# Kernel optimization log

Hardware: AMD Instinct MI355X
Metric: run time of the kernel (lower is better)

## Reference

```python
import jax, jax.numpy as jnp
import numpy as np

MARGIN = 1.0
REL_W = 0.3


def setup_inputs() -> dict:
    key = jax.random.key(0)
    ks = jax.random.split(key, 12)
    D = 256
    inp = {
        'support': jax.random.normal(ks[0], (16, 5, 1, 2, D), jnp.float32),
        'support_negative': jax.random.normal(ks[1], (16, 5, 1, 2, D), jnp.float32),
        'query': jax.random.normal(ks[2], (16, 128, 1, 2, D), jnp.float32),
        'negative': jax.random.normal(ks[3], (16, 128, 1, 2, D), jnp.float32),
        # PatternLearner conv weights (kaiming-ish scale), squeezed to 2-D since all convs are (1,3)/(1,1)
        'w1': jax.random.normal(ks[4], (128, 3), jnp.float32) * np.float32(np.sqrt(2.0 / 3.0)),
        'b1': jnp.zeros((128,), jnp.float32),
        'w2': jax.random.normal(ks[5], (64, 128), jnp.float32) * np.float32(np.sqrt(2.0 / 128.0)),
        'b2': jnp.zeros((64,), jnp.float32),
        'w3': jax.random.normal(ks[6], (32, 64), jnp.float32) * np.float32(np.sqrt(2.0 / 64.0)),
        'b3': jnp.zeros((32,), jnp.float32),
        'w4': jax.random.normal(ks[7], (1, 32), jnp.float32) * np.float32(np.sqrt(2.0 / 32.0)),
        'b4': jnp.zeros((1,), jnp.float32),
    }
    return inp


def _pattern_learner(x, w1, b1, w2, b2, w3, b3, w4, b4):
    # x: [B, N, 1, 3, D] -> torch does view+transpose -> conv2d(1,3) over the length-3 axis,
    # then 1x1 channel convs; equivalent to per-(n,d) contractions.
    h = x[:, :, 0]                                   # [B, N, 3, D]
    h = jnp.einsum('bnld,ol->bndo', h, w1) + b1      # [B, N, D, 128]
    h = jax.nn.relu(h)
    h = jax.nn.relu(jnp.einsum('bndi,oi->bndo', h, w2) + b2)
    h = jax.nn.relu(jnp.einsum('bndi,oi->bndo', h, w3) + b3)
    h = jnp.einsum('bndi,oi->bndo', h, w4) + b4      # [B, N, D, 1]
    return h[..., 0]                                 # [B, N, D]


def _concat_relation(pairs, rel):
    # pairs: [B, N, 1, 2, D]; rel: [B, 1, 1, 1, D]
    B, N, C, _, D = pairs.shape
    head = pairs[:, :, :, 0, :]
    tail = pairs[:, :, :, 1, :]
    relb = jnp.broadcast_to(rel[:, :, :, 0, :], (B, N, C, D))
    # torch cat order (relation, head, tail) then reindex [1,0,2] -> (head, relation, tail)
    return jnp.stack([head, relb, tail], axis=3)     # [B, N, 1, 3, D]


def _pattern_match(q, s):
    # q: [B, Nq, D], s: [B, 1, D] -> -L2 norm
    return -jnp.linalg.norm(q - s, axis=-1)


def reference(support, support_negative, query, negative, w1, b1, w2, b2, w3, b3, w4, b4):
    B, num_q = query.shape[0], query.shape[1]
    num_n = negative.shape[1]
    # get_relation(mean=True): tail - head averaged over the few support pairs
    rel = jnp.mean(support[:, :, :, 1, :] - support[:, :, :, 0, :], axis=1, keepdims=True)
    rel = rel[:, :, :, None, :]                      # [B, 1, 1, 1, D]

    sup_t = _concat_relation(support, rel)
    supn_t = _concat_relation(support_negative, rel)
    qry_t = _concat_relation(query, rel)
    neg_t = _concat_relation(negative, rel)

    pl = lambda x: _pattern_learner(x, w1, b1, w2, b2, w3, b3, w4, b4)
    spt_pos = pl(sup_t)                              # [B, few, D]
    spt_neg = pl(supn_t)                             # [B, num_sn, D]
    qry = pl(jnp.concatenate([qry_t, neg_t], axis=1))  # [B, num_q+num_n, D]

    # aggregator == 'relation': prototypes are per-task means of positive support patterns
    proto = jnp.mean(spt_pos, axis=1)                # [B, D]
    spt_pos_m = proto[:, None, :]                    # [B, 1, D]
    spt_neg_m = jnp.mean(spt_neg, axis=1, keepdims=True)

    qry_pos = _pattern_match(qry, spt_pos_m)         # [B, Nq]
    qry_neg = _pattern_match(qry, spt_neg_m)

    # relation_score (vectorized): mean L2 distance to all OTHER tasks' prototypes, negated
    dists = jnp.linalg.norm(qry[:, :, None, :] - proto[None, None, :, :], axis=-1)  # [B, Nq, B]
    idx = jnp.arange(B)
    self_d = dists[idx, :, idx]                      # [B, Nq]
    relation_score = -(dists.sum(-1) - self_d) / (B - 1)

    # margin loss on the true-query slice
    pos_score = _pattern_match(qry[:, :num_q], spt_pos_m)
    neg_score = _pattern_match(qry[:, :num_q], spt_neg_m)
    pos_ = jnp.mean(pos_score)
    neg_ = jnp.mean(neg_score)
    delta_loss = jnp.maximum(0.0, pos_ - neg_ + MARGIN)

    score = jnp.stack([qry_pos, qry_neg], axis=-1).reshape(-1, 2)
    row = jnp.concatenate([jnp.zeros((num_q,), jnp.int32), jnp.ones((num_n,), jnp.int32)])
    y_query = jnp.broadcast_to(row, (B, num_q + num_n)).reshape(-1)

    delta = qry_pos - qry_neg - REL_W * relation_score  # vbm + relation branch
    p_score = delta[:, :num_q]
    n_score = delta[:, num_q:]
    return (score, y_query, p_score, n_score, delta_loss)
```

## Files before the change

### kernel.cpp

```cpp
#include <hip/hip_runtime.h>
#include <hip/hip_bf16.h>

typedef _Float16 f16;
typedef f16 f16x8 __attribute__((ext_vector_type(8)));
typedef f16 f16x2 __attribute__((ext_vector_type(2)));
typedef float f32x4 __attribute__((ext_vector_type(4)));
typedef unsigned int u32;

#define MFMA16(a, b, c) __builtin_amdgcn_mfma_f32_16x16x32_f16((a), (b), (c), 0, 0, 0)

__device__ __forceinline__ u32 pkrz(float a, float b) {
    auto r = __builtin_amdgcn_cvt_pkrtz(a, b);
    return __builtin_bit_cast(u32, r);
}
__device__ __forceinline__ u32 pkmax0(u32 x) {
    f16x2 h = __builtin_bit_cast(f16x2, x);
    f16x2 z = {(f16)0.f, (f16)0.f};
    f16x2 m = __builtin_elementwise_max(h, z);
    return __builtin_bit_cast(u32, m);
}
__device__ __forceinline__ u32 pkrelu(float a, float b) {
    return pkmax0(pkrz(a, b));
}

union U8 { f16x8 h; u32 w[4]; };

#define OFF_Y      4096
#define OFF_PROTO  1093632
#define OFF_SNEG   1097728

__device__ __forceinline__ int b_of(int e) {
    if (e < 20480) return e / 1280;
    if (e < 40960) return (e - 20480) / 1280;
    return (e - 40960) >> 16;
}

__global__ __launch_bounds__(256, 2) void k_main(
    const float* __restrict__ sup, const float* __restrict__ supn,
    const float* __restrict__ qry, const float* __restrict__ neg,
    const float* __restrict__ w1, const float* __restrict__ b1p,
    const float* __restrict__ w2, const float* __restrict__ w3,
    const float* __restrict__ w4, const float* __restrict__ b2p,
    const float* __restrict__ b3p, const float* __restrict__ b4p,
    float* __restrict__ ws)
{
    __shared__ __align__(16) f16x8 w2lds[16 * 64];
    __shared__ __align__(16) f16x8 wpk[13 * 64];
    __shared__ uint2 stage[4][64];
    __shared__ float relb[2][256];
    float* wsY = ws + OFF_Y;

    int tid = threadIdx.x, wv = tid >> 6, lane = tid & 63;
    int g = lane >> 4, col = lane & 15;
    const f32x4 zero4 = {0.f, 0.f, 0.f, 0.f};

    int blkbase = blockIdx.x * 1024;
    int rb0 = b_of(blkbase), rb1 = b_of(blkbase + 1023);

    #pragma unroll
    for (int k = 0; k < 2; k++) {
        int bb = k ? rb1 : rb0;
        float acc = 0.f;
        #pragma unroll
        for (int n = 0; n < 5; n++) {
            const float* base = sup + ((bb * 5 + n) * 2) * 256 + tid;
            acc += base[256] - base[0];
        }
        relb[k][tid] = acc * 0.2f;
    }

    #pragma unroll
    for (int i = 0; i < 4; i++) {
        int id = tid + 256 * i;
        int f = id >> 6, ln = id & 63;
        int gg = ln >> 4, cr = ln & 15;
        int t = f >> 2, kk = f & 3, out = t * 16 + cr;
        U8 v;
        #pragma unroll
        for (int i2 = 0; i2 < 8; i2++) {
            int u = (2 * kk + (i2 >> 2)) * 16 + gg * 4 + (i2 & 3);
            v.h[i2] = (f16)w2[out * 128 + u];
        }
        w2lds[id] = v.h;
    }
    for (int id = tid; id < 13 * 64; id += 256) {
        int fi = id >> 6, ln = id & 63;
        int gg = ln >> 4, cr = ln & 15, kb = gg * 8;
        U8 v;
        if (fi < 8) {
            int out = fi * 16 + cr;
            #pragma unroll
            for (int i2 = 0; i2 < 8; i2++) {
                int k = kb + i2;
                v.h[i2] = (f16)((k < 3) ? w1[out * 3 + k] : (k == 3 ? b1p[out] : 0.f));
            }
        } else if (fi < 12) {
            int f = fi - 8; int t = f >> 1, kk = f & 1; int out = t * 16 + cr;
            #pragma unroll
            for (int i2 = 0; i2 < 8; i2++) {
                int u = (2 * kk + (i2 >> 2)) * 16 + gg * 4 + (i2 & 3);
                v.h[i2] = (f16)w3[out * 64 + u];
            }
        } else {
            #pragma unroll
            for (int i2 = 0; i2 < 8; i2++) {
                int u = (i2 >> 2) * 16 + gg * 4 + (i2 & 3);
                v.h[i2] = (f16)((cr == 0) ? w4[u] : 0.f);
            }
        }
        wpk[id] = v.h;
    }
    __syncthreads();

    f16x8 w1f[8], w3f[4], w4f;
    #pragma unroll
    for (int f = 0; f < 8; f++) w1f[f] = wpk[f * 64 + lane];
    #pragma unroll
    for (int f = 0; f < 4; f++) w3f[f] = wpk[(8 + f) * 64 + lane];
    w4f = wpk[12 * 64 + lane];

    f32x4 bias2[4], bias3[2];
    #pragma unroll
    for (int t = 0; t < 4; t++) {
        int o = t * 16 + g * 4;
        bias2[t] = (f32x4){b2p[o], b2p[o + 1], b2p[o + 2], b2p[o + 3]};
    }
    #pragma unroll
    for (int t = 0; t < 2; t++) {
        int o = t * 16 + g * 4;
        bias3[t] = (f32x4){b3p[o], b3p[o + 1], b3p[o + 2], b3p[o + 3]};
    }
    float b4v = b4p[0];

    int base = blkbase + wv * 256;

    for (int it = 0; it < 4; ++it) {
        int e = base + it * 64 + lane;
        const float* hp; int bb, dd;
        if (e < 40960) {
            int e2 = (e < 20480) ? e : e - 20480;
            bb = e2 / 1280; int r = e2 - bb * 1280;
            int n = r >> 8; dd = r & 255;
            const float* srcp = (e < 20480) ? sup : supn;
            hp = srcp + ((bb * 5 + n) * 2) * 256 + dd;
        } else {
            int e2 = e - 40960;
            bb = e2 >> 16; int r = e2 & 65535, m = r >> 8; dd = r & 255;
            hp = (m < 128) ? (qry + ((bb * 128 + m) * 2) * 256 + dd)
                           : (neg + ((bb * 128 + (m - 128)) * 2) * 256 + dd);
        }
        float x0 = hp[0], x2 = hp[256];
        float x1 = relb[(bb == rb0) ? 0 : 1][dd];
        stage[wv][lane] = make_uint2(pkrz(x0, x1), pkrz(x2, 1.0f));

        #pragma unroll
        for (int jp = 0; jp < 2; ++jp) {
            U8 b1a, b1b;
            #pragma unroll
            for (int q = 0; q < 4; q++) { b1a.w[q] = 0u; b1b.w[q] = 0u; }
            if (g == 0) {
                uint2 sa = stage[wv][(2 * jp) * 16 + col];
                uint2 sb = stage[wv][(2 * jp + 1) * 16 + col];
                b1a.w[0] = sa.x; b1a.w[1] = sa.y;
                b1b.w[0] = sb.x; b1b.w[1] = sb.y;
            }

            f32x4 c1a[8], c1b[8];
            #pragma unroll
            for (int t = 0; t < 8; t++) {
                c1a[t] = MFMA16(w1f[t], b1a.h, zero4);
                c1b[t] = MFMA16(w1f[t], b1b.h, zero4);
            }

            U8 b2fa[4], b2fb[4];
            #pragma unroll
            for (int kk = 0; kk < 4; kk++) {
                b2fa[kk].w[0] = pkrelu(c1a[2 * kk][0],     c1a[2 * kk][1]);
                b2fa[kk].w[1] = pkrelu(c1a[2 * kk][2],     c1a[2 * kk][3]);
                b2fa[kk].w[2] = pkrelu(c1a[2 * kk + 1][0], c1a[2 * kk + 1][1]);
                b2fa[kk].w[3] = pkrelu(c1a[2 * kk + 1][2], c1a[2 * kk + 1][3]);
                b2fb[kk].w[0] = pkrelu(c1b[2 * kk][0],     c1b[2 * kk][1]);
                b2fb[kk].w[1] = pkrelu(c1b[2 * kk][2],     c1b[2 * kk][3]);
                b2fb[kk].w[2] = pkrelu(c1b[2 * kk + 1][0], c1b[2 * kk + 1][1]);
                b2fb[kk].w[3] = pkrelu(c1b[2 * kk + 1][2], c1b[2 * kk + 1][3]);
            }

            f32x4 c2a[4], c2b[4];
            #pragma unroll
            for (int t = 0; t < 4; t++) {
                f32x4 ca = bias2[t], cb = bias2[t];
                #pragma unroll
                for (int kk = 0; kk < 4; kk++) {
                    f16x8 wfr = w2lds[(t * 4 + kk) * 64 + lane];
                    ca = MFMA16(wfr, b2fa[kk].h, ca);
                    cb = MFMA16(wfr, b2fb[kk].h, cb);
                }
                c2a[t] = ca; c2b[t] = cb;
            }

            U8 b3fa[2], b3fb[2];
            #pragma unroll
            for (int kk = 0; kk < 2; kk++) {
                b3fa[kk].w[0] = pkrelu(c2a[2 * kk][0],     c2a[2 * kk][1]);
                b3fa[kk].w[1] = pkrelu(c2a[2 * kk][2],     c2a[2 * kk][3]);
                b3fa[kk].w[2] = pkrelu(c2a[2 * kk + 1][0], c2a[2 * kk + 1][1]);
                b3fa[kk].w[3] = pkrelu(c2a[2 * kk + 1][2], c2a[2 * kk + 1][3]);
                b3fb[kk].w[0] = pkrelu(c2b[2 * kk][0],     c2b[2 * kk][1]);
                b3fb[kk].w[1] = pkrelu(c2b[2 * kk][2],     c2b[2 * kk][3]);
                b3fb[kk].w[2] = pkrelu(c2b[2 * kk + 1][0], c2b[2 * kk + 1][1]);
                b3fb[kk].w[3] = pkrelu(c2b[2 * kk + 1][2], c2b[2 * kk + 1][3]);
            }

            f32x4 c3a[2], c3b[2];
            #pragma unroll
            for (int t = 0; t < 2; t++) {
                f32x4 ca = bias3[t], cb = bias3[t];
                #pragma unroll
                for (int kk = 0; kk < 2; kk++) {
                    ca = MFMA16(w3f[t * 2 + kk], b3fa[kk].h, ca);
                    cb = MFMA16(w3f[t * 2 + kk], b3fb[kk].h, cb);
                }
                c3a[t] = ca; c3b[t] = cb;
            }

            U8 b4fa, b4fb;
            b4fa.w[0] = pkrelu(c3a[0][0], c3a[0][1]);
            b4fa.w[1] = pkrelu(c3a[0][2], c3a[0][3]);
            b4fa.w[2] = pkrelu(c3a[1][0], c3a[1][1]);
            b4fa.w[3] = pkrelu(c3a[1][2], c3a[1][3]);
            b4fb.w[0] = pkrelu(c3b[0][0], c3b[0][1]);
            b4fb.w[1] = pkrelu(c3b[0][2], c3b[0][3]);
            b4fb.w[2] = pkrelu(c3b[1][0], c3b[1][1]);
            b4fb.w[3] = pkrelu(c3b[1][2], c3b[1][3]);

            f32x4 c4a = MFMA16(w4f, b4fa.h, zero4);
            f32x4 c4b = MFMA16(w4f, b4fb.h, zero4);
            if (lane < 16) {
                wsY[base + it * 64 + (2 * jp) * 16 + lane]     = c4a[0] + b4v;
                wsY[base + it * 64 + (2 * jp + 1) * 16 + lane] = c4b[0] + b4v;
            }
        }
    }
}

__global__ void k_means(float* __restrict__ ws)
{
    int idx = blockIdx.x * 256 + threadIdx.x;
    int b = idx >> 8, d = idx & 255;
    const float* y = ws + OFF_Y;
    float sp = 0.f, sn = 0.f;
    #pragma unroll
    for (int n = 0; n < 5; n++) {
        sp += y[b * 1280 + n * 256 + d];
        sn += y[20480 + b * 1280 + n * 256 + d];
    }
    ws[OFF_PROTO + idx] = sp * 0.2f;
    ws[OFF_SNEG + idx] = sn * 0.2f;
}

__global__ __launch_bounds__(256) void k_scores(float* __restrict__ ws, float* __restrict__ out)
{
    __shared__ float proto[16][256];
    __shared__ float snegs[256];
    const float* y = ws + OFF_Y;
    int tid = threadIdx.x;
    int row0 = blockIdx.x * 16;
    int b = row0 >> 8;

    #pragma unroll
    for (int i = 0; i < 16; i++)
        proto[i][tid] = ws[OFF_PROTO + i * 256 + tid];
    snegs[tid] = ws[OFF_SNEG + b * 256 + tid];
    __syncthreads();

    int wv = tid >> 6, lane = tid & 63;

    for (int r = 0; r < 4; r++) {
        int row = row0 + wv * 4 + r;
        int m = row & 255;
        const float* q = y + 40960 + row * 256;
        float q0 = q[lane], q1 = q[lane + 64], q2 = q[lane + 128], q3 = q[lane + 192];

        float s[17];
        #pragma unroll
        for (int c = 0; c < 16; c++) {
            float d0 = q0 - proto[c][lane],       d1 = q1 - proto[c][lane + 64];
            float d2 = q2 - proto[c][lane + 128], d3 = q3 - proto[c][lane + 192];
            s[c] = d0 * d0 + d1 * d1 + d2 * d2 + d3 * d3;
        }
        {
            float d0 = q0 - snegs[lane],       d1 = q1 - snegs[lane + 64];
            float d2 = q2 - snegs[lane + 128], d3 = q3 - snegs[lane + 192];
            s[16] = d0 * d0 + d1 * d1 + d2 * d2 + d3 * d3;
        }
        #pragma unroll
        for (int off = 32; off > 0; off >>= 1) {
            #pragma unroll
            for (int c = 0; c < 17; c++) s[c] += __shfl_xor(s[c], off, 64);
        }
        float sumd = 0.f, selfd = 0.f;
        #pragma unroll
        for (int c = 0; c < 16; c++) {
            float dc = sqrtf(s[c]);
            sumd += dc;
            if (c == b) selfd = dc;
        }
        float qpos = -selfd;
        float qneg = -sqrtf(s[16]);
        float relation = -(sumd - selfd) * (1.f / 15.f);
        float delta = qpos - qneg - 0.3f * relation;

        if (lane == 0) {
            out[2 * row] = qpos;
            out[2 * row + 1] = qneg;
            out[8192 + row] = (m < 128) ? 0.f : 1.f;
            if (m < 128) out[12288 + b * 128 + m] = delta;
            else         out[14336 + b * 128 + (m - 128)] = delta;
        }
    }
}

__global__ __launch_bounds__(256) void k_final(float* __restrict__ out)
{
    __shared__ float red[2][256];
    int t = threadIdx.x;
    float sp = 0.f, sn = 0.f;
    #pragma unroll
    for (int i = 0; i < 8; i++) {
        int idx = t + 256 * i;
        int b = idx >> 7, m = idx & 127;
        int row = b * 256 + m;
        sp += out[2 * row];
        sn += out[2 * row + 1];
    }
    red[0][t] = sp; red[1][t] = sn;
    __syncthreads();
    #pragma unroll
    for (int off = 128; off > 0; off >>= 1) {
        if (t < off) { red[0][t] += red[0][t + off]; red[1][t] += red[1][t + off]; }
        __syncthreads();
    }
    if (t == 0) {
        float v = (red[0][0] - red[1][0]) * (1.f / 2048.f) + 1.f;
        out[16384] = fmaxf(v, 0.f);
    }
}

extern "C" void kernel_launch(void* const* d_in, const int* in_sizes, int n_in,
                              void* d_out, int out_size, void* d_ws, size_t ws_size,
                              hipStream_t stream)
{
    const float* sup  = (const float*)d_in[0];
    const float* supn = (const float*)d_in[1];
    const float* qry  = (const float*)d_in[2];
    const float* neg  = (const float*)d_in[3];
    const float* w1   = (const float*)d_in[4];
    const float* b1   = (const float*)d_in[5];
    const float* w2   = (const float*)d_in[6];
    const float* b2   = (const float*)d_in[7];
    const float* w3   = (const float*)d_in[8];
    const float* b3   = (const float*)d_in[9];
    const float* w4   = (const float*)d_in[10];
    const float* b4   = (const float*)d_in[11];
    float* ws  = (float*)d_ws;
    float* out = (float*)d_out;

    k_main  <<<1064, 256, 0, stream>>>(sup, supn, qry, neg, w1, b1, w2, w3, w4, b2, b3, b4, ws);
    k_means <<<16,   256, 0, stream>>>(ws);
    k_scores<<<256,  256, 0, stream>>>(ws, out);
    k_final <<<1,    256, 0, stream>>>(out);
}
```

Baseline: 133.4 us.

## Hoist weight packing and relation mean into a separate prep kernel

Adds a k_prep kernel that computes the per-task relation mean once and packs all conv weights into f16 MFMA fragment layout in the workspace. k_main then loads the prepacked fragments directly instead of every one of its 1064 blocks redoing the scattered fp32 weight gathers, conversions and the relation mean. The cost is one extra kernel launch plus a workspace round trip, and x1 is now read from global memory rather than LDS. The launch_bounds(256,2) hint is also dropped from k_main.

```diff
diff --git a/kernel.cpp b/kernel.cpp
--- a/kernel.cpp
+++ b/kernel.cpp
@@ -25,99 +25,95 @@
 
 union U8 { f16x8 h; u32 w[4]; };
 
+#define OFF_REL    0
 #define OFF_Y      4096
 #define OFF_PROTO  1093632
 #define OFF_SNEG   1097728
-
-__device__ __forceinline__ int b_of(int e) {
-    if (e < 20480) return e / 1280;
-    if (e < 40960) return (e - 20480) / 1280;
-    return (e - 40960) >> 16;
-}
-
-__global__ __launch_bounds__(256, 2) void k_main(
+#define OFF_W      1101828
+
+__global__ void k_prep(const float* __restrict__ sup, const float* __restrict__ supn,
+                       const float* __restrict__ w1, const float* __restrict__ b1,
+                       const float* __restrict__ w2, const float* __restrict__ w3,
+                       const float* __restrict__ w4, float* __restrict__ ws)
+{
+    int tid = threadIdx.x;
+    if (blockIdx.x < 16) {
+        int idx = blockIdx.x * 256 + tid;
+        int b = idx >> 8, d = idx & 255;
+        float acc = 0.f;
+        #pragma unroll
+        for (int n = 0; n < 5; n++) {
+            const float* base = sup + ((b * 5 + n) * 2) * 256 + d;
+            acc += base[256] - base[0];
+        }
+        ws[OFF_REL + idx] = acc * 0.2f;
+    } else {
+        f16* wf = (f16*)(ws + OFF_W);
+        for (int id = tid; id < 29 * 64; id += 256) {
+            int frag = id >> 6, lane = id & 63;
+            int g = lane >> 4, cr = lane & 15, kb = g * 8;
+            float vals[8];
+            if (frag < 8) {
+                int out = frag * 16 + cr;
+                #pragma unroll
+                for (int i = 0; i < 8; i++) {
+                    int k = kb + i;
+                    vals[i] = (k < 3) ? w1[out * 3 + k] : (k == 3 ? b1[out] : 0.f);
+                }
+            } else if (frag < 24) {
+                int f = frag - 8; int t = f >> 2, kk = f & 3; int out = t * 16 + cr;
+                #pragma unroll
+                for (int i = 0; i < 8; i++) {
+                    int u = (2 * kk + (i >> 2)) * 16 + g * 4 + (i & 3);
+                    vals[i] = w2[out * 128 + u];
+                }
+            } else if (frag < 28) {
+                int f = frag - 24; int t = f >> 1, kk = f & 1; int out = t * 16 + cr;
+                #pragma unroll
+                for (int i = 0; i < 8; i++) {
+                    int u = (2 * kk + (i >> 2)) * 16 + g * 4 + (i & 3);
+                    vals[i] = w3[out * 64 + u];
+                }
+            } else {
+                #pragma unroll
+                for (int i = 0; i < 8; i++) {
+                    int u = (i >> 2) * 16 + g * 4 + (i & 3);
+                    vals[i] = (cr == 0) ? w4[u] : 0.f;
+                }
+            }
+            #pragma unroll
+            for (int i = 0; i < 8; i++) wf[id * 8 + i] = (f16)vals[i];
+        }
+    }
+}
+
+__global__ void k_main(
     const float* __restrict__ sup, const float* __restrict__ supn,
     const float* __restrict__ qry, const float* __restrict__ neg,
-    const float* __restrict__ w1, const float* __restrict__ b1p,
-    const float* __restrict__ w2, const float* __restrict__ w3,
-    const float* __restrict__ w4, const float* __restrict__ b2p,
-    const float* __restrict__ b3p, const float* __restrict__ b4p,
-    float* __restrict__ ws)
+    const float* __restrict__ b2p, const float* __restrict__ b3p,
+    const float* __restrict__ b4p, float* __restrict__ ws)
 {
     __shared__ __align__(16) f16x8 w2lds[16 * 64];
-    __shared__ __align__(16) f16x8 wpk[13 * 64];
     __shared__ uint2 stage[4][64];
-    __shared__ float relb[2][256];
+    const float* wsRel = ws + OFF_REL;
     float* wsY = ws + OFF_Y;
+    const f16x8* wf = (const f16x8*)(ws + OFF_W);
 
     int tid = threadIdx.x, wv = tid >> 6, lane = tid & 63;
     int g = lane >> 4, col = lane & 15;
     const f32x4 zero4 = {0.f, 0.f, 0.f, 0.f};
 
-    int blkbase = blockIdx.x * 1024;
-    int rb0 = b_of(blkbase), rb1 = b_of(blkbase + 1023);
-
-    #pragma unroll
-    for (int k = 0; k < 2; k++) {
-        int bb = k ? rb1 : rb0;
-        float acc = 0.f;
-        #pragma unroll
-        for (int n = 0; n < 5; n++) {
-            const float* base = sup + ((bb * 5 + n) * 2) * 256 + tid;
-            acc += base[256] - base[0];
-        }
-        relb[k][tid] = acc * 0.2f;
-    }
-
     #pragma unroll
     for (int i = 0; i < 4; i++) {
         int id = tid + 256 * i;
-        int f = id >> 6, ln = id & 63;
-        int gg = ln >> 4, cr = ln & 15;
-        int t = f >> 2, kk = f & 3, out = t * 16 + cr;
-        U8 v;
-        #pragma unroll
-        for (int i2 = 0; i2 < 8; i2++) {
-            int u = (2 * kk + (i2 >> 2)) * 16 + gg * 4 + (i2 & 3);
-            v.h[i2] = (f16)w2[out * 128 + u];
-        }
-        w2lds[id] = v.h;
-    }
-    for (int id = tid; id < 13 * 64; id += 256) {
-        int fi = id >> 6, ln = id & 63;
-        int gg = ln >> 4, cr = ln & 15, kb = gg * 8;
-        U8 v;
-        if (fi < 8) {
-            int out = fi * 16 + cr;
-            #pragma unroll
-            for (int i2 = 0; i2 < 8; i2++) {
-                int k = kb + i2;
-                v.h[i2] = (f16)((k < 3) ? w1[out * 3 + k] : (k == 3 ? b1p[out] : 0.f));
-            }
-        } else if (fi < 12) {
-            int f = fi - 8; int t = f >> 1, kk = f & 1; int out = t * 16 + cr;
-            #pragma unroll
-            for (int i2 = 0; i2 < 8; i2++) {
-                int u = (2 * kk + (i2 >> 2)) * 16 + gg * 4 + (i2 & 3);
-                v.h[i2] = (f16)w3[out * 64 + u];
-            }
-        } else {
-            #pragma unroll
-            for (int i2 = 0; i2 < 8; i2++) {
-                int u = (i2 >> 2) * 16 + gg * 4 + (i2 & 3);
-                v.h[i2] = (f16)((cr == 0) ? w4[u] : 0.f);
-            }
-        }
-        wpk[id] = v.h;
-    }
-    __syncthreads();
-
+        w2lds[id] = wf[8 * 64 + id];
+    }
     f16x8 w1f[8], w3f[4], w4f;
     #pragma unroll
-    for (int f = 0; f < 8; f++) w1f[f] = wpk[f * 64 + lane];
-    #pragma unroll
-    for (int f = 0; f < 4; f++) w3f[f] = wpk[(8 + f) * 64 + lane];
-    w4f = wpk[12 * 64 + lane];
+    for (int f = 0; f < 8; f++) w1f[f] = wf[f * 64 + lane];
+    #pragma unroll
+    for (int f = 0; f < 4; f++) w3f[f] = wf[(24 + f) * 64 + lane];
+    w4f = wf[28 * 64 + lane];
 
     f32x4 bias2[4], bias3[2];
     #pragma unroll
@@ -132,25 +128,28 @@
     }
     float b4v = b4p[0];
 
-    int base = blkbase + wv * 256;
+    __syncthreads();
+
+    int base = blockIdx.x * 1024 + wv * 256;
 
     for (int it = 0; it < 4; ++it) {
         int e = base + it * 64 + lane;
-        const float* hp; int bb, dd;
+        const float* hp; int bd;
         if (e < 40960) {
             int e2 = (e < 20480) ? e : e - 20480;
-            bb = e2 / 1280; int r = e2 - bb * 1280;
-            int n = r >> 8; dd = r & 255;
+            int b = e2 / 1280; int r = e2 - b * 1280;
+            int n = r >> 8, d = r & 255;
             const float* srcp = (e < 20480) ? sup : supn;
-            hp = srcp + ((bb * 5 + n) * 2) * 256 + dd;
+            hp = srcp + ((b * 5 + n) * 2) * 256 + d;
+            bd = b * 256 + d;
         } else {
             int e2 = e - 40960;
-            bb = e2 >> 16; int r = e2 & 65535, m = r >> 8; dd = r & 255;
-            hp = (m < 128) ? (qry + ((bb * 128 + m) * 2) * 256 + dd)
-                           : (neg + ((bb * 128 + (m - 128)) * 2) * 256 + dd);
-        }
-        float x0 = hp[0], x2 = hp[256];
-        float x1 = relb[(bb == rb0) ? 0 : 1][dd];
+            int b = e2 >> 16, r = e2 & 65535, m = r >> 8, d = r & 255;
+            hp = (m < 128) ? (qry + ((b * 128 + m) * 2) * 256 + d)
+                           : (neg + ((b * 128 + (m - 128)) * 2) * 256 + d);
+            bd = b * 256 + d;
+        }
+        float x0 = hp[0], x2 = hp[256], x1 = wsRel[bd];
         stage[wv][lane] = make_uint2(pkrz(x0, x1), pkrz(x2, 1.0f));
 
         #pragma unroll
@@ -365,7 +364,8 @@
     float* ws  = (float*)d_ws;
     float* out = (float*)d_out;
 
-    k_main  <<<1064, 256, 0, stream>>>(sup, supn, qry, neg, w1, b1, w2, w3, w4, b2, b3, b4, ws);
+    k_prep  <<<17,   256, 0, stream>>>(sup, supn, w1, b1, w2, w3, w4, ws);
+    k_main  <<<1064, 256, 0, stream>>>(sup, supn, qry, neg, b2, b3, b4, ws);
     k_means <<<16,   256, 0, stream>>>(ws);
     k_scores<<<256,  256, 0, stream>>>(ws, out);
     k_final <<<1,    256, 0, stream>>>(out);
```

Result: slower. 248.3 us (+86.1%).
